# Kernel optimization log

Hardware: AMD Instinct MI355X
Metric: run time of the kernel (lower is better)

Reference implementation:

```python
import jax, jax.numpy as jnp
import numpy as np

B, N, F_IN = 32, 512, 64
HEADS = (8, 8)
HIDS = (64, 64)
EDGE_P = 0.05  # graph density
NEG_SLOPE = 0.2
NEG_INF = -1e20


def setup_inputs() -> dict:
    key = jax.random.key(0)
    ks = jax.random.split(key, 8)
    x = jax.random.normal(ks[0], (B, N, F_IN), dtype=jnp.float32)
    adj = (jax.random.uniform(ks[1], (B, N, N)) < EDGE_P).astype(jnp.float32)
    adj = jnp.maximum(adj, adj.transpose(0, 2, 1))  # symmetric adjacency
    # mask = (batch, row): every (b, n) pair gets the masked softmax
    b_idx = jnp.repeat(jnp.arange(B, dtype=jnp.int32), N)   # [B*N]
    r_idx = jnp.tile(jnp.arange(N, dtype=jnp.int32), B)     # [B*N]
    # layer 0: f_in=64 -> f_out=64, H=8 ; layer 1: f_in=64*8=512 -> f_out=64, H=8
    W0 = jax.random.normal(ks[2], (F_IN, HIDS[0]), dtype=jnp.float32) / jnp.sqrt(jnp.float32(F_IN))
    a_src0 = jax.random.normal(ks[3], (HIDS[0], HEADS[0]), dtype=jnp.float32) / jnp.sqrt(jnp.float32(HIDS[0]))
    a_dst0 = jax.random.normal(ks[4], (HIDS[0], HEADS[0]), dtype=jnp.float32) / jnp.sqrt(jnp.float32(HIDS[0]))
    f_in1 = HIDS[0] * HEADS[0]
    W1 = jax.random.normal(ks[5], (f_in1, HIDS[1]), dtype=jnp.float32) / jnp.sqrt(jnp.float32(f_in1))
    a_src1 = jax.random.normal(ks[6], (HIDS[1], HEADS[1]), dtype=jnp.float32) / jnp.sqrt(jnp.float32(HIDS[1]))
    a_dst1 = jax.random.normal(ks[7], (HIDS[1], HEADS[1]), dtype=jnp.float32) / jnp.sqrt(jnp.float32(HIDS[1]))
    return dict(x=x, adj=adj, b_idx=b_idx, r_idx=r_idx,
                W0=W0, a_src0=a_src0, a_dst0=a_dst0,
                W1=W1, a_src1=a_src1, a_dst1=a_dst1)


def _gat_layer(x, adj, b_idx, r_idx, W, a_src, a_dst):
    # x: [B,N,f_in], adj: [B,N,N] (diag already set), W: [f_in,F], a_*: [F,H]
    hp = x @ W                                        # [B,N,F]
    s = jnp.einsum('bnf,fh->bhn', hp, a_src)          # attn_src
    d = jnp.einsum('bnf,fh->bhn', hp, a_dst)          # attn_dst
    attn = s[:, :, :, None] + d[:, :, None, :]        # [B,H,N,N]
    attn = jnp.where(attn >= 0, attn, NEG_SLOPE * attn)  # leaky_relu(0.2)
    attn = jnp.where(adj[:, None, :, :] == 0, 0.0, attn)  # masked_fill(adj==0, 0)
    rows = attn[b_idx, :, r_idx, :]                   # [K,H,N]
    rows = jnp.where(rows == 0.0, NEG_INF, rows)
    rows = jax.nn.softmax(rows, axis=-1)
    attn = attn.at[b_idx, :, r_idx, :].set(rows)
    return jnp.einsum('bhij,bjf->bhif', attn, hp)     # [B,H,N,F]


def reference(x, adj, b_idx, r_idx, W0, a_src0, a_dst0, W1, a_src1, a_dst1):
    Bn, Nn = x.shape[:2]
    # torch mutates adj in place: adj[batch,row,row] = 1 (self loops)
    adj = adj.at[b_idx, r_idx, r_idx].set(1.0)
    o = _gat_layer(x, adj, b_idx, r_idx, W0, a_src0, a_dst0)      # [B,H,N,F0]
    x1 = jax.nn.elu(o.transpose(0, 2, 1, 3).reshape(Bn, Nn, -1))  # [B,N,H*F0]
    o2 = _gat_layer(x1, adj, b_idx, r_idx, W1, a_src1, a_dst1)    # [B,H,N,F1]
    return o2.mean(axis=1)                                        # [B,N,F1]
```

## Files before the change

### kernel.cpp

```cpp
#include <hip/hip_runtime.h>
#include <hip/hip_bf16.h>
#include <math.h>

#define BB 32
#define NN 512

typedef _Float16 f16x8 __attribute__((ext_vector_type(8)));
typedef __fp16  fp16x2 __attribute__((ext_vector_type(2)));
typedef float f32x4 __attribute__((ext_vector_type(4)));

#define MFMA16(a, b, c) __builtin_amdgcn_mfma_f32_16x16x32_f16(a, b, c, 0, 0, 0)

union AF { f16x8 v; unsigned int u[4]; };

__device__ __forceinline__ void gload_lds16(const void* g, void* l) {
    __builtin_amdgcn_global_load_lds(
        (const __attribute__((address_space(1))) unsigned int*)g,
        (__attribute__((address_space(3))) unsigned int*)l, 16, 0, 0);
}
__device__ __forceinline__ void gload_lds4(const void* g, void* l) {
    __builtin_amdgcn_global_load_lds(
        (const __attribute__((address_space(1))) unsigned int*)g,
        (__attribute__((address_space(3))) unsigned int*)l, 4, 0, 0);
}

static __device__ __forceinline__ void epi16(
    const float* ctile, const float* asd_f, int row0, int t,
    float* __restrict__ s, float* __restrict__ dTg, _Float16* __restrict__ hpT,
    float* dmax_lds, float* __restrict__ pmax_out)
{
    int b = row0 >> 9, jb = row0 & 511;
    if (t < 128) {
        int rr = t >> 3, h = t & 7;
        float sv = 0.f, dv = 0.f;
#pragma unroll
        for (int f = 0; f < 64; ++f) {
            float hv = ctile[rr * 66 + f];
            sv = fmaf(hv, asd_f[f * 8 + h], sv);
            dv = fmaf(hv, asd_f[512 + f * 8 + h], dv);
        }
        s[((size_t)b * NN + jb + rr) * 8 + h] = sv;
        dTg[((size_t)b * 8 + h) * NN + jb + rr] = dv;
        dmax_lds[t] = dv;
    } else if (t < 256) {
        int t2 = t - 128;
        int f = t2 >> 1, jl = (t2 & 1) * 8;
        f16x8 hv;
#pragma unroll
        for (int e = 0; e < 8; ++e)
            hv[e] = (_Float16)ctile[(jl + e) * 66 + f];
        *(f16x8*)(hpT + ((size_t)b * 64 + f) * NN + jb + jl) = hv;
    }
    __syncthreads();
    if (t < 8) {
        float m = dmax_lds[t];
#pragma unroll
        for (int k = 1; k < 16; ++k) m = fmaxf(m, dmax_lds[t + 8 * k]);
        pmax_out[((size_t)b * 32 + (jb >> 4)) * 8 + t] = m;
    }
}

static __device__ __forceinline__ void epi32(
    const float* ctile, const float* asd_f, int row0, int t,
    float* __restrict__ s, float* __restrict__ dTg, _Float16* __restrict__ hpT,
    float* dmax_lds, float* __restrict__ pmax_out)
{
    int b = row0 >> 9, jb = row0 & 511;
    if (t < 256) {
        int rr = t >> 3, h = t & 7;
        float sv = 0.f, dv = 0.f;
#pragma unroll
        for (int f = 0; f < 64; ++f) {
            float hv = ctile[rr * 66 + f];
            sv = fmaf(hv, asd_f[f * 8 + h], sv);
            dv = fmaf(hv, asd_f[512 + f * 8 + h], dv);
        }
        s[((size_t)b * NN + jb + rr) * 8 + h] = sv;
        dTg[((size_t)b * 8 + h) * NN + jb + rr] = dv;
        dmax_lds[t] = dv;
    } else {
        int t2 = t - 256;
        int f = t2 >> 2, jl = (t2 & 3) * 8;
        f16x8 hv;
#pragma unroll
        for (int e = 0; e < 8; ++e)
            hv[e] = (_Float16)ctile[(jl + e) * 66 + f];
        *(f16x8*)(hpT + ((size_t)b * 64 + f) * NN + jb + jl) = hv;
    }
    __syncthreads();
    if (t < 8) {
        float m = dmax_lds[t];
#pragma unroll
        for (int k = 1; k < 32; ++k) m = fmaxf(m, dmax_lds[t + 8 * k]);
        pmax_out[((size_t)b * 16 + (jb >> 5)) * 8 + t] = m;
    }
}

__global__ __launch_bounds__(256) void k_front(
    const float* __restrict__ x, const float* __restrict__ W0,
    const float* __restrict__ W1, _Float16* __restrict__ W1T,
    const float* __restrict__ a_src, const float* __restrict__ a_dst,
    const float* __restrict__ adj, unsigned long long* __restrict__ adjb,
    float* __restrict__ s, float* __restrict__ dTg, _Float16* __restrict__ hpT,
    float* __restrict__ pmax)
{
    __shared__ float ctile[16 * 66];
    __shared__ float asd_f[1024];
    __shared__ unsigned int mrow[16][16];
    __shared__ float dmax[128];
    int t = threadIdx.x, row0 = blockIdx.x * 16;
    int lane = t & 63, w = t >> 6, cn = lane & 15, rq = lane >> 4;

    if (blockIdx.x < 16) {
        int task = blockIdx.x * 256 + t;
        int n = task & 63, gabs = task >> 6;
        int c = gabs >> 3, g = gabs & 7;
        f16x8 hv;
#pragma unroll
        for (int e = 0; e < 8; ++e)
            hv[e] = (_Float16)W1[(size_t)(gabs * 8 + e) * 64 + n];
        *(f16x8*)(W1T + (size_t)n * 512 + c * 64 + (g ^ (n & 7)) * 8) = hv;
    }

    int ar = t >> 4, seg = t & 15;
    const float* ap = adj + (size_t)(row0 + ar) * NN + seg * 32;
    float4 av[8];
#pragma unroll
    for (int q = 0; q < 8; ++q) av[q] = ((const float4*)ap)[q];

    ((float4*)asd_f)[t] = (t < 128) ? ((const float4*)a_src)[t]
                                    : ((const float4*)a_dst)[t - 128];
    f32x4 acc;
#pragma unroll
    for (int e = 0; e < 4; ++e) acc[e] = 0.f;
    int nn0 = w * 16 + cn;
#pragma unroll
    for (int ks = 0; ks < 2; ++ks) {
        const float* xp = x + (size_t)(row0 + cn) * 64 + ks * 32 + rq * 8;
        float4 x0 = *(const float4*)xp, x1 = *(const float4*)(xp + 4);
        f16x8 ah = {(_Float16)x0.x, (_Float16)x0.y, (_Float16)x0.z, (_Float16)x0.w,
                    (_Float16)x1.x, (_Float16)x1.y, (_Float16)x1.z, (_Float16)x1.w};
        f16x8 bh;
#pragma unroll
        for (int e = 0; e < 8; ++e)
            bh[e] = (_Float16)W0[(size_t)((ks * 4 + rq) * 8 + e) * 64 + nn0];
        acc = MFMA16(ah, bh, acc);
    }
#pragma unroll
    for (int r = 0; r < 4; ++r)
        ctile[(rq * 4 + r) * 66 + w * 16 + cn] = acc[r];
    __syncthreads();
    epi16(ctile, asd_f, row0, t, s, dTg, hpT, dmax, pmax);

    unsigned int m32 = 0;
#pragma unroll
    for (int q = 0; q < 8; ++q) {
        if (av[q].x != 0.f) m32 |= 1u << (q * 4 + 0);
        if (av[q].y != 0.f) m32 |= 1u << (q * 4 + 1);
        if (av[q].z != 0.f) m32 |= 1u << (q * 4 + 2);
        if (av[q].w != 0.f) m32 |= 1u << (q * 4 + 3);
    }
    int i = (row0 + ar) & (NN - 1);
    if ((i >> 5) == seg) m32 |= 1u << (i & 31);
    mrow[ar][seg] = m32;
    __syncthreads();
    if (t < 128) {
        int r = t >> 3, k = t & 7;
        unsigned long long u = (unsigned long long)mrow[r][2 * k]
                             | ((unsigned long long)mrow[r][2 * k + 1] << 32);
        adjb[(size_t)(row0 + r) * 8 + k] = u;
    }
}

#define PBUILD(AOUT, SV, M_, MBYTE, DDv)                                \
    do {                                                                \
        _Pragma("unroll")                                               \
        for (int e = 0; e < 8; e += 2) {                                \
            float pA[2];                                                \
            _Pragma("unroll")                                           \
            for (int q = 0; q < 2; ++q) {                               \
                int ee = e + q;                                         \
                bool con = (MBYTE >> ee) & 1u;                          \
                float e0 = SV + DDv[ee];                                \
                float l0 = fmaxf(e0, 0.2f * e0);                        \
                float p0 = __expf(l0 - M_);                             \
                pA[q] = (con && l0 != 0.f) ? p0 : 0.f;                  \
            }                                                           \
            fp16x2 ka = __builtin_amdgcn_cvt_pkrtz(pA[0], pA[1]);       \
            AOUT.u[e >> 1] = __builtin_bit_cast(unsigned int, ka);      \
        }                                                               \
    } while (0)

template<int MODE>
__global__ __launch_bounds__(512, 4) void k_attn_fused(
    const unsigned long long* __restrict__ adjb, const float* __restrict__ s,
    const float* __restrict__ dTg, const float* __restrict__ pmaxd,
    const _Float16* __restrict__ hpT,
    const _Float16* __restrict__ W1T,
    const float* __restrict__ a_src, const float* __restrict__ a_dst,
    float* __restrict__ s_out, float* __restrict__ dTg_out,
    _Float16* __restrict__ hpT_out, float* __restrict__ pmax_out,
    float* __restrict__ o_f)
{
    __shared__ __align__(16) char smem[38400];
    char* bufP = smem;
    char* bufQ = smem + 10240;

    int blk = blockIdx.x;
    int vb = ((blk & 7) << 6) | (blk >> 3);
    int b = vb >> 4, i0 = (vb & 15) << 5;
    int row0 = vb * 32;
    int t = threadIdx.x, lane = t & 63, w = t >> 6;
    int cn = lane & 15, rq = lane >> 4;
    int myrow = i0 + cn;

    const _Float16* hb = hpT + (size_t)b * 64 * NN;
    int f0 = t >> 3, g0 = t & 7;
    const _Float16* hsrc = hb + (size_t)f0 * NN + ((g0 ^ (f0 & 7)) * 8);
    const float* dsrc = dTg + ((size_t)b * 8 + w) * NN + lane;

    {
        gload_lds16(hsrc, (_Float16*)bufP + (w << 9));
        gload_lds4(dsrc, (float*)(bufP + 8192) + (w << 6));
    }

    constexpr int NT = (MODE == 0) ? 32 : 16;
    float md = pmaxd[((size_t)b * NT + (lane & (NT - 1))) * 8 + w];
#pragma unroll
    for (int off = NT >> 1; off; off >>= 1) md = fmaxf(md, __shfl_xor(md, off));

    float svA = s[((size_t)b * NN + myrow) * 8 + w];
    float svB = s[((size_t)b * NN + myrow + 16) * 8 + w];
    float MA = fmaxf(svA + md, 0.f);
    float MB = fmaxf(svB + md, 0.f);
    const unsigned long long* abr = adjb + ((size_t)b * NN + myrow) * 8;
    int rq8 = rq * 8;

    f16x8 ones;
#pragma unroll
    for (int e = 0; e < 8; ++e) ones[e] = (_Float16)1.0f;

    f32x4 accA[4], accB[4], accrsA, accrsB;
#pragma unroll
    for (int e = 0; e < 4; ++e) { accrsA[e] = 0.f; accrsB[e] = 0.f; }
#pragma unroll
    for (int ft = 0; ft < 4; ++ft)
#pragma unroll
        for (int e = 0; e < 4; ++e) { accA[ft][e] = 0.f; accB[ft][e] = 0.f; }

    unsigned long long mbA = abr[0], mbB = abr[128];
    __syncthreads();

    for (int jcx = 0; jcx < 8; ++jcx) {
        int jc = jcx * 64;
        char* cur = (jcx & 1) ? bufQ : bufP;
        char* nxt = (jcx & 1) ? bufP : bufQ;
        if (jcx < 7) {
            gload_lds16(hsrc + jc + 64, (_Float16*)nxt + (w << 9));
            gload_lds4(dsrc + jc + 64, (float*)(nxt + 8192) + (w << 6));
        }
        unsigned long long mbnA = (jcx < 7) ? abr[jcx + 1] : 0ull;
        unsigned long long mbnB = (jcx < 7) ? abr[jcx + 129] : 0ull;
        const _Float16* hTc = (const _Float16*)cur;
        const float* ddl = (const float*)(cur + 8192) + (w << 6);
        unsigned int mlA = (unsigned)mbA, mhA = (unsigned)(mbA >> 32);
        unsigned int mlB = (unsigned)mbB, mhB = (unsigned)(mbB >> 32);
#pragma unroll
        for (int ks = 0; ks < 2; ++ks) {
            float dd[8];
            *(float4*)&dd[0] = *(const float4*)(ddl + ks * 32 + rq8);
            *(float4*)&dd[4] = *(const float4*)(ddl + ks * 32 + rq8 + 4);
            unsigned int mbyA = ((ks ? mhA : mlA) >> rq8) & 0xffu;
            unsigned int mbyB = ((ks ? mhB : mlB) >> rq8) & 0xffu;
            AF aA, aB;
            PBUILD(aA, svA, MA, mbyA, dd);
            PBUILD(aB, svB, MB, mbyB, dd);
            accrsA = MFMA16(aA.v, ones, accrsA);
            accrsB = MFMA16(aB.v, ones, accrsB);
#pragma unroll
            for (int ft = 0; ft < 4; ++ft) {
                int f = ft * 16 + cn;
                f16x8 bh = *(const f16x8*)&hTc[f * 64 + (((ks * 4 + rq) ^ (f & 7)) * 8)];
                accA[ft] = MFMA16(aA.v, bh, accA[ft]);
                accB[ft] = MFMA16(aB.v, bh, accB[ft]);
            }
        }
        mbA = mbnA; mbB = mbnB;
        __syncthreads();
    }

    float invrA[4], invrB[4];
#pragma unroll
    for (int r = 0; r < 4; ++r) {
        invrA[r] = 1.0f / accrsA[r];
        invrB[r] = 1.0f / accrsB[r];
    }

    if (MODE == 0) {
        _Float16* x1all = (_Float16*)smem;
#pragma unroll
        for (int rt = 0; rt < 2; ++rt)
#pragma unroll
            for (int ft = 0; ft < 4; ++ft)
#pragma unroll
                for (int r = 0; r < 4; ++r) {
                    int il = rt * 16 + rq * 4 + r;
                    float v = rt ? accB[ft][r] * invrB[r]
                                 : accA[ft][r] * invrA[r];
                    v = v > 0.f ? v : __expf(v) - 1.f;
                    int f = ft * 16 + cn;
                    x1all[w * 2048 + il * 64 + (((f >> 3) ^ (il & 7)) * 8) + (f & 7)] =
                        (_Float16)v;
                }
        __syncthreads();
        f32x4 g1A, g1B;
#pragma unroll
        for (int e = 0; e < 4; ++e) { g1A[e] = 0.f; g1B[e] = 0.f; }
        int nn = (w & 3) * 16 + cn, kh = w >> 2;
        const _Float16* wb = W1T + (size_t)nn * 512;
#pragma unroll
        for (int kc2 = 0; kc2 < 4; ++kc2) {
            int kc = kh * 4 + kc2;
#pragma unroll
            for (int ks = 0; ks < 2; ++ks) {
                f16x8 bh = *(const f16x8*)(wb + kc * 64 +
                                           (((ks * 4 + rq) ^ (nn & 7)) * 8));
                f16x8 ahA = *(const f16x8*)&x1all[kc * 2048 + cn * 64 +
                                                  (((ks * 4 + rq) ^ (cn & 7)) * 8)];
                f16x8 ahB = *(const f16x8*)&x1all[kc * 2048 + (16 + cn) * 64 +
                                                  (((ks * 4 + rq) ^ (cn & 7)) * 8)];
                g1A = MFMA16(ahA, bh, g1A);
                g1B = MFMA16(ahB, bh, g1B);
            }
        }
        __syncthreads();
        float* ct = (float*)smem;
        float* asd_f = (float*)(smem + 33280);
        float* dmax = (float*)(smem + 37376);
#pragma unroll
        for (int r = 0; r < 4; ++r) {
            ct[kh * 2112 + (rq * 4 + r) * 66 + nn] = g1A[r];
            ct[kh * 2112 + (16 + rq * 4 + r) * 66 + nn] = g1B[r];
        }
        if (t < 256)
            ((float4*)asd_f)[t] = (t < 128) ? ((const float4*)a_src)[t]
                                            : ((const float4*)a_dst)[t - 128];
        __syncthreads();
        for (int idx = t; idx < 2112; idx += 512) ct[idx] += ct[2112 + idx];
        __syncthreads();
        epi32(ct, asd_f, row0, t, s_out, dTg_out, hpT_out, dmax, pmax_out);
    } else {
        float* red = (float*)smem;
#pragma unroll
        for (int ph = 0; ph < 2; ++ph) {
            if ((w >> 2) == ph) {
#pragma unroll
                for (int rt = 0; rt < 2; ++rt)
#pragma unroll
                    for (int ft = 0; ft < 4; ++ft)
#pragma unroll
                        for (int r = 0; r < 4; ++r) {
                            int il = rt * 16 + rq * 4 + r;
                            float v = rt ? accB[ft][r] * invrB[r]
                                         : accA[ft][r] * invrA[r];
                            int off = (w & 3) * 2048 + il * 64 + ft * 16 + cn;
                            if (ph == 0) red[off] = v;
                            else         red[off] += v;
                        }
            }
            __syncthreads();
        }
#pragma unroll
        for (int u = 0; u < 4; ++u) {
            int idx = t + u * 512;
            int il = idx >> 6, f = idx & 63;
            float sum = red[il * 64 + f] + red[2048 + il * 64 + f]
                      + red[4096 + il * 64 + f] + red[6144 + il * 64 + f];
            o_f[((size_t)b * NN + i0 + il) * 64 + f] = sum * 0.125f;
        }
    }
}

extern "C" void kernel_launch(void* const* d_in, const int* in_sizes, int n_in,
                              void* d_out, int out_size, void* d_ws, size_t ws_size,
                              hipStream_t stream) {
    const float* x      = (const float*)d_in[0];
    const float* adj    = (const float*)d_in[1];
    const float* W0     = (const float*)d_in[4];
    const float* a_src0 = (const float*)d_in[5];
    const float* a_dst0 = (const float*)d_in[6];
    const float* W1     = (const float*)d_in[7];
    const float* a_src1 = (const float*)d_in[8];
    const float* a_dst1 = (const float*)d_in[9];
    float* out = (float*)d_out;

    float* ws = (float*)d_ws;
    const size_t R = (size_t)BB * NN;
    const size_t BHN = (size_t)BB * 8 * NN;
    float* s0    = ws;
    float* dTg0  = s0 + R * 8;
    float* s1    = dTg0 + BHN;
    float* dTg1  = s1 + R * 8;
    float* pmax0 = dTg1 + BHN;
    float* pmax1 = pmax0 + 8192;
    _Float16* hp0T = (_Float16*)(pmax1 + 4096);
    _Float16* hp1T = hp0T + (size_t)BB * 64 * NN;
    _Float16* W1T  = hp1T + (size_t)BB * 64 * NN;
    unsigned long long* adjb = (unsigned long long*)(W1T + (size_t)64 * 512);

    k_front<<<1024, 256, 0, stream>>>(x, W0, W1, W1T, a_src0, a_dst0,
                                      adj, adjb, s0, dTg0, hp0T, pmax0);
    k_attn_fused<0><<<512, 512, 0, stream>>>(adjb, s0, dTg0, pmax0, hp0T,
                                             W1T, a_src1, a_dst1,
                                             s1, dTg1, hp1T, pmax1, nullptr);
    k_attn_fused<1><<<512, 512, 0, stream>>>(adjb, s1, dTg1, pmax1, hp1T,
                                             nullptr, nullptr, nullptr,
                                             nullptr, nullptr, nullptr, nullptr, out);
}
```

Before: 160.8 us.

## Stream raw fp32 adjacency into attention kernels instead of precomputed bitmask

Drops the bitmask packing of the adjacency matrix from the front kernel. Both attention kernels now stream fp32 adjacency tiles into LDS (XOR-swizzled) alongside the hp/d tiles in the double-buffered pipeline, and derive connectivity plus the self-loop directly. This removes the extra adjb write/read pass and shortens the front kernel. In exchange, each attention layer reads 32x more adjacency bytes (fp32 instead of bits), and LDS use per buffer roughly doubles.

```diff
diff --git a/kernel.cpp b/kernel.cpp
--- a/kernel.cpp
+++ b/kernel.cpp
@@ -100,13 +100,11 @@
     const float* __restrict__ x, const float* __restrict__ W0,
     const float* __restrict__ W1, _Float16* __restrict__ W1T,
     const float* __restrict__ a_src, const float* __restrict__ a_dst,
-    const float* __restrict__ adj, unsigned long long* __restrict__ adjb,
     float* __restrict__ s, float* __restrict__ dTg, _Float16* __restrict__ hpT,
     float* __restrict__ pmax)
 {
     __shared__ float ctile[16 * 66];
     __shared__ float asd_f[1024];
-    __shared__ unsigned int mrow[16][16];
     __shared__ float dmax[128];
     int t = threadIdx.x, row0 = blockIdx.x * 16;
     int lane = t & 63, w = t >> 6, cn = lane & 15, rq = lane >> 4;
@@ -121,12 +119,6 @@
             hv[e] = (_Float16)W1[(size_t)(gabs * 8 + e) * 64 + n];
         *(f16x8*)(W1T + (size_t)n * 512 + c * 64 + (g ^ (n & 7)) * 8) = hv;
     }
-
-    int ar = t >> 4, seg = t & 15;
-    const float* ap = adj + (size_t)(row0 + ar) * NN + seg * 32;
-    float4 av[8];
-#pragma unroll
-    for (int q = 0; q < 8; ++q) av[q] = ((const float4*)ap)[q];
 
     ((float4*)asd_f)[t] = (t < 128) ? ((const float4*)a_src)[t]
                                     : ((const float4*)a_dst)[t - 128];
@@ -151,28 +143,9 @@
         ctile[(rq * 4 + r) * 66 + w * 16 + cn] = acc[r];
     __syncthreads();
     epi16(ctile, asd_f, row0, t, s, dTg, hpT, dmax, pmax);
-
-    unsigned int m32 = 0;
-#pragma unroll
-    for (int q = 0; q < 8; ++q) {
-        if (av[q].x != 0.f) m32 |= 1u << (q * 4 + 0);
-        if (av[q].y != 0.f) m32 |= 1u << (q * 4 + 1);
-        if (av[q].z != 0.f) m32 |= 1u << (q * 4 + 2);
-        if (av[q].w != 0.f) m32 |= 1u << (q * 4 + 3);
-    }
-    int i = (row0 + ar) & (NN - 1);
-    if ((i >> 5) == seg) m32 |= 1u << (i & 31);
-    mrow[ar][seg] = m32;
-    __syncthreads();
-    if (t < 128) {
-        int r = t >> 3, k = t & 7;
-        unsigned long long u = (unsigned long long)mrow[r][2 * k]
-                             | ((unsigned long long)mrow[r][2 * k + 1] << 32);
-        adjb[(size_t)(row0 + r) * 8 + k] = u;
-    }
-}
-
-#define PBUILD(AOUT, SV, M_, MBYTE, DDv)                                \
+}
+
+#define PBUILD(AOUT, SV, M_, AVv, REL, DDv)                             \
     do {                                                                \
         _Pragma("unroll")                                               \
         for (int e = 0; e < 8; e += 2) {                                \
@@ -180,7 +153,7 @@
             _Pragma("unroll")                                           \
             for (int q = 0; q < 2; ++q) {                               \
                 int ee = e + q;                                         \
-                bool con = (MBYTE >> ee) & 1u;                          \
+                bool con = (AVv[ee] != 0.f) || (ee == (REL));           \
                 float e0 = SV + DDv[ee];                                \
                 float l0 = fmaxf(e0, 0.2f * e0);                        \
                 float p0 = __expf(l0 - M_);                             \
@@ -193,9 +166,9 @@
 
 template<int MODE>
 __global__ __launch_bounds__(512, 4) void k_attn_fused(
-    const unsigned long long* __restrict__ adjb, const float* __restrict__ s,
-    const float* __restrict__ dTg, const float* __restrict__ pmaxd,
-    const _Float16* __restrict__ hpT,
+    const float* __restrict__ s, const float* __restrict__ dTg,
+    const float* __restrict__ pmaxd, const _Float16* __restrict__ hpT,
+    const float* __restrict__ adj,
     const _Float16* __restrict__ W1T,
     const float* __restrict__ a_src, const float* __restrict__ a_dst,
     float* __restrict__ s_out, float* __restrict__ dTg_out,
@@ -204,7 +177,7 @@
 {
     __shared__ __align__(16) char smem[38400];
     char* bufP = smem;
-    char* bufQ = smem + 10240;
+    char* bufQ = smem + 18432;
 
     int blk = blockIdx.x;
     int vb = ((blk & 7) << 6) | (blk >> 3);
@@ -218,11 +191,17 @@
     int f0 = t >> 3, g0 = t & 7;
     const _Float16* hsrc = hb + (size_t)f0 * NN + ((g0 ^ (f0 & 7)) * 8);
     const float* dsrc = dTg + ((size_t)b * 8 + w) * NN + lane;
-
-    {
-        gload_lds16(hsrc, (_Float16*)bufP + (w << 9));
-        gload_lds4(dsrc, (float*)(bufP + 8192) + (w << 6));
-    }
+    int ar = t >> 4, ag = t & 15;
+    const float* asrc = adj + (size_t)(row0 + ar) * NN + (((ag ^ (ar & 7))) << 2);
+
+#define STAGE(BUF, JC)                                                   \
+    do {                                                                 \
+        gload_lds16(hsrc + (JC), (_Float16*)(BUF) + (w << 9));           \
+        gload_lds4(dsrc + (JC), (float*)((BUF) + 8192) + (w << 6));      \
+        gload_lds16(asrc + (JC), (float*)((BUF) + 10240) + (w << 8));    \
+    } while (0)
+
+    STAGE(bufP, 0);
 
     constexpr int NT = (MODE == 0) ? 32 : 16;
     float md = pmaxd[((size_t)b * NT + (lane & (NT - 1))) * 8 + w];
@@ -233,7 +212,6 @@
     float svB = s[((size_t)b * NN + myrow + 16) * 8 + w];
     float MA = fmaxf(svA + md, 0.f);
     float MB = fmaxf(svB + md, 0.f);
-    const unsigned long long* abr = adjb + ((size_t)b * NN + myrow) * 8;
     int rq8 = rq * 8;
 
     f16x8 ones;
@@ -248,33 +226,35 @@
 #pragma unroll
         for (int e = 0; e < 4; ++e) { accA[ft][e] = 0.f; accB[ft][e] = 0.f; }
 
-    unsigned long long mbA = abr[0], mbB = abr[128];
     __syncthreads();
 
     for (int jcx = 0; jcx < 8; ++jcx) {
         int jc = jcx * 64;
         char* cur = (jcx & 1) ? bufQ : bufP;
         char* nxt = (jcx & 1) ? bufP : bufQ;
-        if (jcx < 7) {
-            gload_lds16(hsrc + jc + 64, (_Float16*)nxt + (w << 9));
-            gload_lds4(dsrc + jc + 64, (float*)(nxt + 8192) + (w << 6));
-        }
-        unsigned long long mbnA = (jcx < 7) ? abr[jcx + 1] : 0ull;
-        unsigned long long mbnB = (jcx < 7) ? abr[jcx + 129] : 0ull;
+        if (jcx < 7) STAGE(nxt, jc + 64);
         const _Float16* hTc = (const _Float16*)cur;
         const float* ddl = (const float*)(cur + 8192) + (w << 6);
-        unsigned int mlA = (unsigned)mbA, mhA = (unsigned)(mbA >> 32);
-        unsigned int mlB = (unsigned)mbB, mhB = (unsigned)(mbB >> 32);
+        const float* adl = (const float*)(cur + 10240);
+        const float* arA = adl + cn * 64;
+        const float* arB = adl + (16 + cn) * 64;
+        int xA = cn & 7;
 #pragma unroll
         for (int ks = 0; ks < 2; ++ks) {
-            float dd[8];
-            *(float4*)&dd[0] = *(const float4*)(ddl + ks * 32 + rq8);
-            *(float4*)&dd[4] = *(const float4*)(ddl + ks * 32 + rq8 + 4);
-            unsigned int mbyA = ((ks ? mhA : mlA) >> rq8) & 0xffu;
-            unsigned int mbyB = ((ks ? mhB : mlB) >> rq8) & 0xffu;
+            int jo = ks * 32 + rq8;
+            float dd[8], avA[8], avB[8];
+            *(float4*)&dd[0] = *(const float4*)(ddl + jo);
+            *(float4*)&dd[4] = *(const float4*)(ddl + jo + 4);
+            int G0 = jo >> 2;
+            *(float4*)&avA[0] = *(const float4*)(arA + ((G0 ^ xA) << 2));
+            *(float4*)&avA[4] = *(const float4*)(arA + (((G0 + 1) ^ xA) << 2));
+            *(float4*)&avB[0] = *(const float4*)(arB + ((G0 ^ xA) << 2));
+            *(float4*)&avB[4] = *(const float4*)(arB + (((G0 + 1) ^ xA) << 2));
+            int relA = myrow - (jc + jo);
+            int relB = relA + 16;
             AF aA, aB;
-            PBUILD(aA, svA, MA, mbyA, dd);
-            PBUILD(aB, svB, MB, mbyB, dd);
+            PBUILD(aA, svA, MA, avA, relA, dd);
+            PBUILD(aB, svB, MB, avB, relB, dd);
             accrsA = MFMA16(aA.v, ones, accrsA);
             accrsB = MFMA16(aB.v, ones, accrsB);
 #pragma unroll
@@ -285,9 +265,9 @@
                 accB[ft] = MFMA16(aB.v, bh, accB[ft]);
             }
         }
-        mbA = mbnA; mbB = mbnB;
-        __syncthreads();
-    }
+        __syncthreads();
+    }
+#undef STAGE
 
     float invrA[4], invrB[4];
 #pragma unroll
@@ -406,14 +386,13 @@
     _Float16* hp0T = (_Float16*)(pmax1 + 4096);
     _Float16* hp1T = hp0T + (size_t)BB * 64 * NN;
     _Float16* W1T  = hp1T + (size_t)BB * 64 * NN;
-    unsigned long long* adjb = (unsigned long long*)(W1T + (size_t)64 * 512);
 
     k_front<<<1024, 256, 0, stream>>>(x, W0, W1, W1T, a_src0, a_dst0,
-                                      adj, adjb, s0, dTg0, hp0T, pmax0);
-    k_attn_fused<0><<<512, 512, 0, stream>>>(adjb, s0, dTg0, pmax0, hp0T,
+                                      s0, dTg0, hp0T, pmax0);
+    k_attn_fused<0><<<512, 512, 0, stream>>>(s0, dTg0, pmax0, hp0T, adj,
                                              W1T, a_src1, a_dst1,
                                              s1, dTg1, hp1T, pmax1, nullptr);
-    k_attn_fused<1><<<512, 512, 0, stream>>>(adjb, s1, dTg1, pmax1, hp1T,
+    k_attn_fused<1><<<512, 512, 0, stream>>>(s1, dTg1, pmax1, hp1T, adj,
                                              nullptr, nullptr, nullptr,
                                              nullptr, nullptr, nullptr, nullptr, out);
 }
```

New measurement: 155.7 us. 3.2% less time.
